# Optimization experiments

Hardware: AMD Instinct MI355X
Metric: run time of the kernel (lower is better)

## Reference

```python
import jax, jax.numpy as jnp
import numpy as np

EPS = 1e-12  # matches torch F.normalize eps clamp


def _l2norm(v, axis):
    n = jnp.sqrt(jnp.sum(v * v, axis=axis, keepdims=True))
    return v / jnp.maximum(n, EPS)


def setup_inputs() -> dict:
    key = jax.random.key(0)
    k1, k2, k3, k4 = jax.random.split(key, 4)
    N, C, H, W, K = 64, 128, 64, 64, 64
    x = jax.random.normal(k1, (N, C, H, W), dtype=jnp.float32)
    conv_w = jax.random.normal(k2, (K, C), dtype=jnp.float32) * 0.1  # 1x1 conv weight squeezed
    conv_b = jax.random.normal(k3, (K,), dtype=jnp.float32) * 0.1
    centroids = jax.random.uniform(k4, (K, C), dtype=jnp.float32)
    return {"x": x, "conv_w": conv_w, "conv_b": conv_b, "centroids": centroids}


def reference(x, conv_w, conv_b, centroids):
    N, C = x.shape[:2]
    K = centroids.shape[0]
    xf = x.reshape(N, C, -1)                                   # (N, C, P) with P = H*W
    # 1x1 conv == per-pixel linear map over channels
    logits = jnp.einsum('ncp,kc->nkp', xf, conv_w) + conv_b[None, :, None]
    a = jax.nn.softmax(logits, axis=1)                         # soft assignment over clusters
    # vlad[n,k,c] = sum_p a[n,k,p] * (x[n,c,p] - centroids[k,c])
    vlad = jnp.einsum('nkp,ncp->nkc', a, xf) \
        - jnp.sum(a, axis=-1)[:, :, None] * centroids[None]    # (N, K, C)
    vlad = _l2norm(vlad, axis=2)                               # intra-cluster normalization
    vlad = vlad.reshape(N, K * C)
    return _l2norm(vlad, axis=1)
```

## Files before the change

### kernel.cpp

```cpp
#include <hip/hip_runtime.h>
#include <math.h>

#define NNIMG 64
#define CCH 128
#define KK 64
#define PP 4096
#define BSPLIT 16
#define PB (PP / BSPLIT)
#define PC 32
#define NCHUNK (PB / PC)

typedef __attribute__((ext_vector_type(8))) short short8;
typedef __attribute__((ext_vector_type(4))) float f32x4;

__device__ __forceinline__ unsigned short bf16_rtne(float f) {
  unsigned u = __float_as_uint(f);
  unsigned r = u + 0x7FFFu + ((u >> 16) & 1u);
  return (unsigned short)(r >> 16);
}
__device__ __forceinline__ float bf16_tof(unsigned short h) {
  return __uint_as_float(((unsigned)h) << 16);
}

__device__ __forceinline__ void lgkm_barrier() {
  __asm__ volatile("s_waitcnt lgkmcnt(0)\n\ts_barrier" ::: "memory");
}
__device__ __forceinline__ void vm_barrier() {
  __asm__ volatile("s_waitcnt vmcnt(0) lgkmcnt(0)\n\ts_barrier" ::: "memory");
}

__device__ __forceinline__ void load_to_lds16(const float* g, float* l) {
  __builtin_amdgcn_global_load_lds((const __attribute__((address_space(1))) void*)g,
                                   (__attribute__((address_space(3))) void*)l, 16, 0, 0);
}

__global__ __launch_bounds__(128, 2) void netvlad_main(
    const float* __restrict__ x, const float* __restrict__ conv_w,
    const float* __restrict__ conv_b, float* __restrict__ vg,
    float* __restrict__ ag) {
  __shared__ __align__(16) float xraw[CCH * PC];
  __shared__ __align__(16) unsigned int pc[PC * 66];
  __shared__ __align__(16) unsigned short a_lds[KK * 40];
  __shared__ float asum_buf[2 * KK];

  const int t = threadIdx.x;
  const int lane = t & 63;
  const int wv = t >> 6;
  const int m = lane & 15;
  const int q = lane >> 4;

  const int n = blockIdx.x >> 4;
  const int blk = blockIdx.x & 15;
  const float* xbase = x + (size_t)n * CCH * PP + blk * PB;

  const int dma_c = (lane >> 3);
  const int dma_p = (lane & 7) * 4;
  auto issue_dma = [&](int ch) {
#pragma unroll
    for (int i = 0; i < 8; ++i) {
      int rowbase = wv * 64 + i * 8;
      const float* g = xbase + (size_t)(rowbase + dma_c) * PP + ch * PC + dma_p;
      load_to_lds16(g, &xraw[rowbase * PC]);
    }
  };

  issue_dma(0);

  short8 Whi[4][4];
#pragma unroll
  for (int kt = 0; kt < 4; ++kt)
#pragma unroll
    for (int cs = 0; cs < 4; ++cs) {
      const float* wp = conv_w + (kt * 16 + m) * CCH + cs * 32 + q * 8;
      float4 wa = *(const float4*)wp;
      float4 wb = *(const float4*)(wp + 4);
      float fv[8] = {wa.x, wa.y, wa.z, wa.w, wb.x, wb.y, wb.z, wb.w};
      short8 h;
#pragma unroll
      for (int j = 0; j < 8; ++j) h[j] = (short)bf16_rtne(fv[j]);
      Whi[kt][cs] = h;
    }
  float b_regs[4][4];
#pragma unroll
  for (int kt = 0; kt < 4; ++kt)
#pragma unroll
    for (int r = 0; r < 4; ++r) b_regs[kt][r] = conv_b[kt * 16 + q * 4 + r];

  f32x4 vacc[4][4];
#pragma unroll
  for (int kt = 0; kt < 4; ++kt)
#pragma unroll
    for (int ct = 0; ct < 4; ++ct) vacc[kt][ct] = (f32x4){0.f, 0.f, 0.f, 0.f};
  float asum_acc[16];
#pragma unroll
  for (int i = 0; i < 16; ++i) asum_acc[i] = 0.f;

  const int sp = lane & 31;
  const int sh = lane >> 5;
  const int prow = wv * 16 + m;
  const unsigned sel_hi = 0x07060302u;
  const unsigned sel_g2 = (m & 1) ? 0x07060302u : 0x05040100u;

#pragma unroll 1
  for (int ch = 0; ch < NCHUNK; ++ch) {
    vm_barrier();

    {
      const float* xr = xraw + (4 * wv + 2 * sh) * PC + sp;
      const int pbase = sp * 66 + 2 * wv + sh;
#pragma unroll
      for (int i = 0; i < 16; ++i) {
        float x0 = xr[i * (8 * PC)];
        float x1 = xr[i * (8 * PC) + PC];
        pc[pbase + 4 * i] =
            __builtin_amdgcn_perm(__float_as_uint(x1), __float_as_uint(x0), sel_hi);
      }
    }
    lgkm_barrier();

    if (ch < NCHUNK - 1) issue_dma(ch + 1);

    f32x4 acc1[4];
#pragma unroll
    for (int kt = 0; kt < 4; ++kt)
      acc1[kt] = (f32x4){b_regs[kt][0], b_regs[kt][1], b_regs[kt][2], b_regs[kt][3]};
    const unsigned int* pcrow = pc + prow * 66;
#pragma unroll
    for (int cs = 0; cs < 4; ++cs) {
      uint2 u01 = *(const uint2*)&pcrow[16 * cs + 4 * q];
      uint2 u23 = *(const uint2*)&pcrow[16 * cs + 4 * q + 2];
      unsigned hs[4] = {u01.x, u01.y, u23.x, u23.y};
      short8 Bf;
      __builtin_memcpy(&Bf, hs, 16);
#pragma unroll
      for (int kt = 0; kt < 4; ++kt)
        acc1[kt] = __builtin_amdgcn_mfma_f32_16x16x32_bf16(Whi[kt][cs], Bf, acc1[kt], 0, 0, 0);
    }

    float ssum = 0.f;
#pragma unroll
    for (int kt = 0; kt < 4; ++kt)
#pragma unroll
      for (int r = 0; r < 4; ++r) {
        float e = __expf(acc1[kt][r]);
        acc1[kt][r] = e;
        ssum += e;
      }
    ssum += __shfl_xor(ssum, 16, 64);
    ssum += __shfl_xor(ssum, 32, 64);
    float inv = 1.0f / ssum;
#pragma unroll
    for (int kt = 0; kt < 4; ++kt)
#pragma unroll
      for (int r = 0; r < 4; ++r) {
        float a = acc1[kt][r] * inv;
        unsigned short h = bf16_rtne(a);
        asum_acc[kt * 4 + r] += bf16_tof(h);
        a_lds[(kt * 16 + q * 4 + r) * 40 + prow] = h;
      }
    lgkm_barrier();

    short8 Af[4];
#pragma unroll
    for (int kt = 0; kt < 4; ++kt)
      Af[kt] = *(const short8*)&a_lds[(kt * 16 + m) * 40 + q * 8];
#pragma unroll
    for (int ct = 0; ct < 4; ++ct) {
      const int ebase = wv * 32 + ct * 8 + (m >> 1);
      unsigned g[8];
#pragma unroll
      for (int j = 0; j < 8; ++j) g[j] = pc[(q * 8 + j) * 66 + ebase];
      unsigned hs[4];
#pragma unroll
      for (int i = 0; i < 4; ++i)
        hs[i] = __builtin_amdgcn_perm(g[2 * i + 1], g[2 * i], sel_g2);
      short8 Bf;
      __builtin_memcpy(&Bf, hs, 16);
#pragma unroll
      for (int kt = 0; kt < 4; ++kt)
        vacc[kt][ct] = __builtin_amdgcn_mfma_f32_16x16x32_bf16(Af[kt], Bf, vacc[kt][ct], 0, 0, 0);
    }
  }

  float* vrow = vg + (size_t)n * (KK * CCH);
#pragma unroll
  for (int kt = 0; kt < 4; ++kt)
#pragma unroll
    for (int ct = 0; ct < 4; ++ct)
#pragma unroll
      for (int r = 0; r < 4; ++r)
        atomicAdd(&vrow[(kt * 16 + q * 4 + r) * CCH + wv * 64 + ct * 16 + m],
                  vacc[kt][ct][r]);
#pragma unroll
  for (int i = 0; i < 16; ++i) {
    float v = asum_acc[i];
    v += __shfl_xor(v, 1, 64);
    v += __shfl_xor(v, 2, 64);
    v += __shfl_xor(v, 4, 64);
    v += __shfl_xor(v, 8, 64);
    if (m == 0) asum_buf[wv * 64 + (i >> 2) * 16 + q * 4 + (i & 3)] = v;
  }
  lgkm_barrier();
  if (t < KK) atomicAdd(&ag[n * KK + t], asum_buf[t] + asum_buf[KK + t]);
}

__global__ __launch_bounds__(256) void netvlad_finish(
    const float* __restrict__ vg, const float* __restrict__ ag,
    const float* __restrict__ centroids, float* __restrict__ out) {
  const int t = threadIdx.x;
  const int w = t >> 6, ln = t & 63;
  const int idx = blockIdx.x * 4 + w;
  const int n = idx >> 6, k = idx & 63;
  const int c = ln * 2;
  float2 v = *(const float2*)&vg[(size_t)(n * KK + k) * CCH + c];
  float s = ag[n * KK + k];
  float2 ce = *(const float2*)&centroids[k * CCH + c];
  float v0 = v.x - s * ce.x;
  float v1 = v.y - s * ce.y;
  float ssq = v0 * v0 + v1 * v1;
#pragma unroll
  for (int off = 32; off > 0; off >>= 1) ssq += __shfl_xor(ssq, off, 64);
  float inv = 0.125f / fmaxf(sqrtf(ssq), 1e-12f);
  float2 o;
  o.x = v0 * inv;
  o.y = v1 * inv;
  *(float2*)&out[(size_t)n * (KK * CCH) + k * CCH + c] = o;
}

extern "C" void kernel_launch(void* const* d_in, const int* in_sizes, int n_in,
                              void* d_out, int out_size, void* d_ws, size_t ws_size,
                              hipStream_t stream) {
  const float* x = (const float*)d_in[0];
  const float* conv_w = (const float*)d_in[1];
  const float* conv_b = (const float*)d_in[2];
  const float* centroids = (const float*)d_in[3];
  float* out = (float*)d_out;

  float* vg = (float*)d_ws;
  float* ag = vg + (size_t)NNIMG * KK * CCH;
  const size_t zbytes = ((size_t)NNIMG * KK * CCH + NNIMG * KK) * sizeof(float);

  hipMemsetAsync(d_ws, 0, zbytes, stream);
  netvlad_main<<<NNIMG * BSPLIT, 128, 0, stream>>>(x, conv_w, conv_b, vg, ag);
  netvlad_finish<<<NNIMG * KK / 4, 256, 0, stream>>>(vg, ag, centroids, out);
}
```

Baseline: 229.4 us.

## Stage whole pixel tile in LDS with triple-buffered DMA and per-block partial outputs

The main kernel now first streams the block's full 256-pixel x slice into a bf16-packed LDS tile using a three-deep global-to-LDS DMA ring with fine-grained vmcnt waits, then runs the two GEMM stages from LDS with 256 threads split into two wave pairs. The pairs combine their accumulators through LDS before writing. When the workspace is large enough, each block writes its partials to its own slot instead of issuing atomics, which also removes the memset, and a new finish kernel sums the 16 partials. This targets per-chunk barrier stalls and atomic contention, at the cost of a large LDS tile that may lower occupancy and of extra global traffic for the partial buffers.

```diff
diff --git a/kernel.cpp b/kernel.cpp
--- a/kernel.cpp
+++ b/kernel.cpp
@@ -6,9 +6,9 @@
 #define KK 64
 #define PP 4096
 #define BSPLIT 16
-#define PB (PP / BSPLIT)
-#define PC 32
-#define NCHUNK (PB / PC)
+#define PB 256
+#define NCHUNK 32
+#define TILE_U32 (PB * 66)
 
 typedef __attribute__((ext_vector_type(8))) short short8;
 typedef __attribute__((ext_vector_type(4))) float f32x4;
@@ -21,27 +21,24 @@
 __device__ __forceinline__ float bf16_tof(unsigned short h) {
   return __uint_as_float(((unsigned)h) << 16);
 }
-
 __device__ __forceinline__ void lgkm_barrier() {
   __asm__ volatile("s_waitcnt lgkmcnt(0)\n\ts_barrier" ::: "memory");
 }
-__device__ __forceinline__ void vm_barrier() {
-  __asm__ volatile("s_waitcnt vmcnt(0) lgkmcnt(0)\n\ts_barrier" ::: "memory");
-}
-
 __device__ __forceinline__ void load_to_lds16(const float* g, float* l) {
   __builtin_amdgcn_global_load_lds((const __attribute__((address_space(1))) void*)g,
                                    (__attribute__((address_space(3))) void*)l, 16, 0, 0);
 }
 
-__global__ __launch_bounds__(128, 2) void netvlad_main(
+template <bool USE_WS>
+__global__ __launch_bounds__(256, 2) void netvlad_main(
     const float* __restrict__ x, const float* __restrict__ conv_w,
-    const float* __restrict__ conv_b, float* __restrict__ vg,
-    float* __restrict__ ag) {
-  __shared__ __align__(16) float xraw[CCH * PC];
-  __shared__ __align__(16) unsigned int pc[PC * 66];
-  __shared__ __align__(16) unsigned short a_lds[KK * 40];
-  __shared__ float asum_buf[2 * KK];
+    const float* __restrict__ conv_b, float* __restrict__ vout,
+    float* __restrict__ aout) {
+  __shared__ __align__(16) unsigned int tile[TILE_U32];
+  __shared__ __align__(16) unsigned char scratch[12288];
+  float* xraw = (float*)scratch;
+  unsigned short* a_lds = (unsigned short*)scratch;
+  float* asum_buf = (float*)(scratch + 10240);
 
   const int t = threadIdx.x;
   const int lane = t & 63;
@@ -53,18 +50,10 @@
   const int blk = blockIdx.x & 15;
   const float* xbase = x + (size_t)n * CCH * PP + blk * PB;
 
-  const int dma_c = (lane >> 3);
-  const int dma_p = (lane & 7) * 4;
-  auto issue_dma = [&](int ch) {
-#pragma unroll
-    for (int i = 0; i < 8; ++i) {
-      int rowbase = wv * 64 + i * 8;
-      const float* g = xbase + (size_t)(rowbase + dma_c) * PP + ch * PC + dma_p;
-      load_to_lds16(g, &xraw[rowbase * PC]);
-    }
+  auto issue_dma = [&](int ch, int buf) {
+    const int c = ch * 4 + wv;
+    load_to_lds16(xbase + (size_t)c * PP + lane * 4, &xraw[buf * 1024 + wv * 256]);
   };
-
-  issue_dma(0);
 
   short8 Whi[4][4];
 #pragma unroll
@@ -85,6 +74,38 @@
   for (int kt = 0; kt < 4; ++kt)
 #pragma unroll
     for (int r = 0; r < 4; ++r) b_regs[kt][r] = conv_b[kt * 16 + q * 4 + r];
+  __asm__ volatile("s_waitcnt vmcnt(0)" ::: "memory");
+
+  issue_dma(0, 0);
+  issue_dma(1, 1);
+  issue_dma(2, 2);
+  const unsigned sel_hi = 0x07060302u;
+
+#pragma unroll 1
+  for (int ch = 0; ch < NCHUNK; ++ch) {
+    if (ch <= NCHUNK - 3)      __asm__ volatile("s_waitcnt vmcnt(2)" ::: "memory");
+    else if (ch == NCHUNK - 2) __asm__ volatile("s_waitcnt vmcnt(1)" ::: "memory");
+    else                       __asm__ volatile("s_waitcnt vmcnt(0)" ::: "memory");
+    __builtin_amdgcn_s_barrier();
+    const int buf = ch % 3;
+    const float* xr = &xraw[buf * 1024];
+    float x0 = xr[t];
+    float x1 = xr[256 + t];
+    float x2 = xr[512 + t];
+    float x3 = xr[768 + t];
+    uint2 w;
+    w.x = __builtin_amdgcn_perm(__float_as_uint(x1), __float_as_uint(x0), sel_hi);
+    w.y = __builtin_amdgcn_perm(__float_as_uint(x3), __float_as_uint(x2), sel_hi);
+    *(uint2*)&tile[t * 66 + 2 * ch] = w;
+    __asm__ volatile("s_waitcnt lgkmcnt(0)" ::: "memory");
+    __builtin_amdgcn_s_barrier();
+    if (ch + 3 < NCHUNK) issue_dma(ch + 3, buf);
+  }
+
+  const int pair = wv >> 1;
+  const int hw = wv & 1;
+  unsigned short* amy = a_lds + pair * (KK * 40);
+  const unsigned sel_g2 = (m & 1) ? 0x07060302u : 0x05040100u;
 
   f32x4 vacc[4][4];
 #pragma unroll
@@ -95,36 +116,16 @@
 #pragma unroll
   for (int i = 0; i < 16; ++i) asum_acc[i] = 0.f;
 
-  const int sp = lane & 31;
-  const int sh = lane >> 5;
-  const int prow = wv * 16 + m;
-  const unsigned sel_hi = 0x07060302u;
-  const unsigned sel_g2 = (m & 1) ? 0x07060302u : 0x05040100u;
-
 #pragma unroll 1
-  for (int ch = 0; ch < NCHUNK; ++ch) {
-    vm_barrier();
-
-    {
-      const float* xr = xraw + (4 * wv + 2 * sh) * PC + sp;
-      const int pbase = sp * 66 + 2 * wv + sh;
-#pragma unroll
-      for (int i = 0; i < 16; ++i) {
-        float x0 = xr[i * (8 * PC)];
-        float x1 = xr[i * (8 * PC) + PC];
-        pc[pbase + 4 * i] =
-            __builtin_amdgcn_perm(__float_as_uint(x1), __float_as_uint(x0), sel_hi);
-      }
-    }
-    lgkm_barrier();
-
-    if (ch < NCHUNK - 1) issue_dma(ch + 1);
+  for (int gi = 0; gi < 4; ++gi) {
+    const int px0 = (pair + 2 * gi) * 32;
+    const int prow = px0 + hw * 16 + m;
 
     f32x4 acc1[4];
 #pragma unroll
     for (int kt = 0; kt < 4; ++kt)
       acc1[kt] = (f32x4){b_regs[kt][0], b_regs[kt][1], b_regs[kt][2], b_regs[kt][3]};
-    const unsigned int* pcrow = pc + prow * 66;
+    const unsigned int* pcrow = tile + prow * 66;
 #pragma unroll
     for (int cs = 0; cs < 4; ++cs) {
       uint2 u01 = *(const uint2*)&pcrow[16 * cs + 4 * q];
@@ -156,41 +157,43 @@
         float a = acc1[kt][r] * inv;
         unsigned short h = bf16_rtne(a);
         asum_acc[kt * 4 + r] += bf16_tof(h);
-        a_lds[(kt * 16 + q * 4 + r) * 40 + prow] = h;
+        amy[(kt * 16 + q * 4 + r) * 40 + hw * 16 + m] = h;
       }
     lgkm_barrier();
 
     short8 Af[4];
 #pragma unroll
     for (int kt = 0; kt < 4; ++kt)
-      Af[kt] = *(const short8*)&a_lds[(kt * 16 + m) * 40 + q * 8];
+      Af[kt] = *(const short8*)&amy[(kt * 16 + m) * 40 + q * 8];
 #pragma unroll
     for (int ct = 0; ct < 4; ++ct) {
-      const int ebase = wv * 32 + ct * 8 + (m >> 1);
+      const int ebase = hw * 32 + ct * 8 + (m >> 1);
       unsigned g[8];
 #pragma unroll
-      for (int j = 0; j < 8; ++j) g[j] = pc[(q * 8 + j) * 66 + ebase];
-      unsigned hs[4];
+      for (int j = 0; j < 8; ++j) g[j] = tile[(px0 + q * 8 + j) * 66 + ebase];
+      unsigned hs2[4];
 #pragma unroll
       for (int i = 0; i < 4; ++i)
-        hs[i] = __builtin_amdgcn_perm(g[2 * i + 1], g[2 * i], sel_g2);
+        hs2[i] = __builtin_amdgcn_perm(g[2 * i + 1], g[2 * i], sel_g2);
       short8 Bf;
-      __builtin_memcpy(&Bf, hs, 16);
+      __builtin_memcpy(&Bf, hs2, 16);
 #pragma unroll
       for (int kt = 0; kt < 4; ++kt)
         vacc[kt][ct] = __builtin_amdgcn_mfma_f32_16x16x32_bf16(Af[kt], Bf, vacc[kt][ct], 0, 0, 0);
     }
-  }
-
-  float* vrow = vg + (size_t)n * (KK * CCH);
-#pragma unroll
-  for (int kt = 0; kt < 4; ++kt)
-#pragma unroll
-    for (int ct = 0; ct < 4; ++ct)
-#pragma unroll
-      for (int r = 0; r < 4; ++r)
-        atomicAdd(&vrow[(kt * 16 + q * 4 + r) * CCH + wv * 64 + ct * 16 + m],
-                  vacc[kt][ct][r]);
+    lgkm_barrier();
+  }
+
+  float* vscr = (float*)tile;
+  if (pair == 1) {
+#pragma unroll
+    for (int kt = 0; kt < 4; ++kt)
+#pragma unroll
+      for (int ct = 0; ct < 4; ++ct)
+#pragma unroll
+        for (int r = 0; r < 4; ++r)
+          vscr[(kt * 16 + q * 4 + r) * CCH + hw * 64 + ct * 16 + m] = vacc[kt][ct][r];
+  }
 #pragma unroll
   for (int i = 0; i < 16; ++i) {
     float v = asum_acc[i];
@@ -201,7 +204,26 @@
     if (m == 0) asum_buf[wv * 64 + (i >> 2) * 16 + q * 4 + (i & 3)] = v;
   }
   lgkm_barrier();
-  if (t < KK) atomicAdd(&ag[n * KK + t], asum_buf[t] + asum_buf[KK + t]);
+  if (pair == 0) {
+    float* vrow = USE_WS ? (vout + (size_t)blockIdx.x * (KK * CCH))
+                         : (vout + (size_t)n * (KK * CCH));
+#pragma unroll
+    for (int kt = 0; kt < 4; ++kt)
+#pragma unroll
+      for (int ct = 0; ct < 4; ++ct)
+#pragma unroll
+        for (int r = 0; r < 4; ++r) {
+          const int idx = (kt * 16 + q * 4 + r) * CCH + hw * 64 + ct * 16 + m;
+          const float v = vacc[kt][ct][r] + vscr[idx];
+          if (USE_WS) vrow[idx] = v;
+          else atomicAdd(&vrow[idx], v);
+        }
+  }
+  if (t < KK) {
+    float s = asum_buf[t] + asum_buf[64 + t] + asum_buf[128 + t] + asum_buf[192 + t];
+    if (USE_WS) aout[blockIdx.x * KK + t] = s;
+    else atomicAdd(&aout[n * KK + t], s);
+  }
 }
 
 __global__ __launch_bounds__(256) void netvlad_finish(
@@ -227,6 +249,36 @@
   *(float2*)&out[(size_t)n * (KK * CCH) + k * CCH + c] = o;
 }
 
+__global__ __launch_bounds__(256) void netvlad_finish_ws(
+    const float* __restrict__ vp, const float* __restrict__ agp,
+    const float* __restrict__ centroids, float* __restrict__ out) {
+  const int t = threadIdx.x;
+  const int w = t >> 6, ln = t & 63;
+  const int idx = blockIdx.x * 4 + w;
+  const int n = idx >> 6, k = idx & 63;
+  const int c = ln * 2;
+  float a0 = 0.f, a1 = 0.f, s = 0.f;
+#pragma unroll
+  for (int b = 0; b < BSPLIT; ++b) {
+    const float* vr = vp + (size_t)(n * BSPLIT + b) * (KK * CCH) + k * CCH + c;
+    float2 v = *(const float2*)vr;
+    a0 += v.x;
+    a1 += v.y;
+    s += agp[(n * BSPLIT + b) * KK + k];
+  }
+  float2 ce = *(const float2*)&centroids[k * CCH + c];
+  float v0 = a0 - s * ce.x;
+  float v1 = a1 - s * ce.y;
+  float ssq = v0 * v0 + v1 * v1;
+#pragma unroll
+  for (int off = 32; off > 0; off >>= 1) ssq += __shfl_xor(ssq, off, 64);
+  float inv = 0.125f / fmaxf(sqrtf(ssq), 1e-12f);
+  float2 o;
+  o.x = v0 * inv;
+  o.y = v1 * inv;
+  *(float2*)&out[(size_t)n * (KK * CCH) + k * CCH + c] = o;
+}
+
 extern "C" void kernel_launch(void* const* d_in, const int* in_sizes, int n_in,
                               void* d_out, int out_size, void* d_ws, size_t ws_size,
                               hipStream_t stream) {
@@ -236,11 +288,20 @@
   const float* centroids = (const float*)d_in[3];
   float* out = (float*)d_out;
 
-  float* vg = (float*)d_ws;
-  float* ag = vg + (size_t)NNIMG * KK * CCH;
-  const size_t zbytes = ((size_t)NNIMG * KK * CCH + NNIMG * KK) * sizeof(float);
-
-  hipMemsetAsync(d_ws, 0, zbytes, stream);
-  netvlad_main<<<NNIMG * BSPLIT, 128, 0, stream>>>(x, conv_w, conv_b, vg, ag);
-  netvlad_finish<<<NNIMG * KK / 4, 256, 0, stream>>>(vg, ag, centroids, out);
-}
+  const size_t WS_NEEDED =
+      ((size_t)NNIMG * BSPLIT * KK * CCH + (size_t)NNIMG * BSPLIT * KK) * sizeof(float);
+
+  if (ws_size >= WS_NEEDED) {
+    float* vp = (float*)d_ws;
+    float* agp = vp + (size_t)NNIMG * BSPLIT * KK * CCH;
+    netvlad_main<true><<<NNIMG * BSPLIT, 256, 0, stream>>>(x, conv_w, conv_b, vp, agp);
+    netvlad_finish_ws<<<NNIMG * KK / 4, 256, 0, stream>>>(vp, agp, centroids, out);
+  } else {
+    float* vg = (float*)d_ws;
+    float* ag = vg + (size_t)NNIMG * KK * CCH;
+    const size_t zbytes = ((size_t)NNIMG * KK * CCH + NNIMG * KK) * sizeof(float);
+    hipMemsetAsync(d_ws, 0, zbytes, stream);
+    netvlad_main<false><<<NNIMG * BSPLIT, 256, 0, stream>>>(x, conv_w, conv_b, vg, ag);
+    netvlad_finish<<<NNIMG * KK / 4, 256, 0, stream>>>(vg, ag, centroids, out);
+  }
+}
```

Result: slower. 242.8 us (+5.8%).
